# Optimization experiments

Hardware: AMD Instinct MI355X
Metric: run time of the kernel (lower is better)

Reference implementation:

```python
import jax, jax.numpy as jnp
import numpy as np

IMG_H, IMG_W = 1024, 1024
STRIDES = (8, 16, 32, 64, 128)
NUM_CLASSES = 80
CONF_THR = 0.05
IOU_THR = 0.5
MAX_PER_CLASS = 100
MAX_DET = 100
K_CAND = 256  # candidates kept per class before greedy NMS (pre-sort cap)


def build_grids():
    gy, gx, gs = [], [], []
    for s in STRIDES:
        H, W = IMG_H // s, IMG_W // s
        h = jnp.arange(H, dtype=jnp.float32)
        w = jnp.arange(W, dtype=jnp.float32)
        gy_, gx_ = jnp.meshgrid(h, w)  # 'xy' indexing -> shape [W, H], matches tf.meshgrid
        gy.append(gy_.reshape(-1))
        gx.append(gx_.reshape(-1))
        gs.append(jnp.full((W * H,), float(s), dtype=jnp.float32))
    return jnp.concatenate(gy), jnp.concatenate(gx), jnp.concatenate(gs)


def pairwise_iou(b):
    # b: [K,4] as (y1, x1, y2, x2)
    y1, x1, y2, x2 = b[:, 0], b[:, 1], b[:, 2], b[:, 3]
    area = (y2 - y1) * (x2 - x1)
    ih = jnp.maximum(jnp.minimum(y2[:, None], y2[None, :]) - jnp.maximum(y1[:, None], y1[None, :]), 0.0)
    iw = jnp.maximum(jnp.minimum(x2[:, None], x2[None, :]) - jnp.maximum(x1[:, None], x1[None, :]), 0.0)
    inter = ih * iw
    union = area[:, None] + area[None, :] - inter
    return inter / jnp.maximum(union, 1e-8)


def nms_one_class(boxes, scores):
    # boxes [N,4], scores [N] -> (sel_boxes [MAX_PER_CLASS,4], sel_scores [MAX_PER_CLASS])
    top_s, idx = jax.lax.top_k(scores, K_CAND)
    cand = boxes[idx]                       # [K,4]
    valid = top_s > CONF_THR
    iou = jax.lax.stop_gradient(pairwise_iou(cand))  # suppression mask is non-differentiable
    rng = jnp.arange(K_CAND)

    def body(i, keep):
        sup = (iou[i] > IOU_THR) & (rng > i) & keep[i]
        return keep & ~sup

    keep = jax.lax.fori_loop(0, K_CAND, body, valid)
    kept = jnp.where(keep, top_s, 0.0)
    sel_s, sel_i = jax.lax.top_k(kept, MAX_PER_CLASS)
    return cand[sel_i], sel_s


def combined_nms(boxes, scores):
    # per image: boxes [N,4] shared across classes, scores [N,C]
    cls_boxes, cls_scores = jax.vmap(nms_one_class, in_axes=(None, 1))(boxes, scores)
    C = scores.shape[1]
    cls_labels = jnp.broadcast_to(jnp.arange(C, dtype=jnp.float32)[:, None], cls_scores.shape)
    flat_s = cls_scores.reshape(-1)
    flat_b = cls_boxes.reshape(-1, 4)
    flat_l = cls_labels.reshape(-1)
    fin_s, fin_i = jax.lax.top_k(flat_s, MAX_DET)
    fin_b = flat_b[fin_i] * (fin_s > 0.0)[:, None].astype(flat_b.dtype)  # zero pad boxes like TF
    fin_l = flat_l[fin_i]
    return fin_b, fin_l, fin_s


def decode(pred_regs, pred_ctrs, pred_clfs):
    gy, gx, gs = build_grids()
    gy, gx, gs = gy[:, None], gx[:, None], gs[:, None]     # [N,1]
    score = pred_clfs * pred_ctrs                           # [B,N,C]
    x1 = gx - pred_regs[..., 0:1]
    x2 = gx + pred_regs[..., 1:2]
    y1 = gy - pred_regs[..., 2:3]
    y2 = gy + pred_regs[..., 3:4]
    bbox = jnp.concatenate([y1, x1, y2, x2], axis=-1) * gs  # [B,N,4] in image coords
    return jax.vmap(combined_nms)(bbox, score)


def setup_inputs() -> dict:
    key = jax.random.key(0)
    k1, k2, k3 = jax.random.split(key, 3)
    N = sum((IMG_H // s) * (IMG_W // s) for s in STRIDES)  # 21824
    B = 16
    return {
        "pred_regs": jax.random.uniform(k1, (B, N, 4), jnp.float32),
        "pred_ctrs": jax.random.uniform(k2, (B, N, 1), jnp.float32),
        "pred_clfs": jax.random.uniform(k3, (B, N, NUM_CLASSES), jnp.float32),
    }


def reference(pred_regs, pred_ctrs, pred_clfs):
    # returns (final_bboxes [B,100,4], final_labels [B,100] float, final_scores [B,100])
    return decode(pred_regs, pred_ctrs, pred_clfs)
```

## Files before the change

### kernel.cpp

```cpp
#include <hip/hip_runtime.h>
#include <stdint.h>

#pragma clang fp contract(off)

namespace {
constexpr int kN = 21824;
constexpr int kB = 16;
constexpr int kC = 80;
constexpr int kK = 256;
constexpr int kMaxPC = 100;
constexpr int kMaxDet = 100;
constexpr int kBins1 = 2048;
constexpr int kCap = 1536;
constexpr int kQCap = 320;
constexpr int kRows = kB * kC;
constexpr int kTiles = kN / 64;
constexpr int kTPB = 6;
constexpr int kGScan = (kTiles + kTPB - 1) / kTPB;
constexpr int kLCap = 48;
constexpr float kThr = 0.72f;
constexpr double kIouC = 0x1.000001p-1;
}

__device__ __forceinline__ uint64_t make_key(float s, int n) {
  return ((uint64_t)__float_as_uint(s) << 16) | (uint32_t)(0xFFFF - n);
}

__device__ uint32_t block_scan_incl(uint32_t val) {
  __shared__ uint32_t wsum[4];
  int lane = threadIdx.x & 63;
  int wave = threadIdx.x >> 6;
  for (int d = 1; d < 64; d <<= 1) {
    uint32_t t = __shfl_up(val, (unsigned)d, 64);
    if (lane >= d) val += t;
  }
  if (lane == 63) wsum[wave] = val;
  __syncthreads();
  uint32_t off = 0;
  for (int w = 0; w < wave; ++w) off += wsum[w];
  __syncthreads();
  return val + off;
}

struct RegSrc {
  uint64_t k[6];
  int cnt;
  template <class F> __device__ void each(F f) const {
    #pragma unroll
    for (int j = 0; j < 6; ++j)
      if (j < cnt) f(k[j]);
  }
};
struct ColSrc {
  const float* cl;
  const float* ct;
  template <class F> __device__ void each(F f) const {
    for (int n = threadIdx.x; n < kN; n += 256)
      f(make_key(cl[(size_t)n * kC] * ct[n], n));
  }
};
struct ArrSrc {
  const float* s;
  int count;
  template <class F> __device__ void each(F f) const {
    for (int i = threadIdx.x; i < count; i += 256) f(make_key(s[i], i));
  }
};

template <class Src>
__device__ int refine_gather(const Src& src, int K, int cap,
                             uint32_t* hist, uint64_t* cbuf) {
  __shared__ int sel_bin;
  __shared__ uint32_t sel_hd, sel_above, qcnt;
  int tid = threadIdx.x;

  for (int i = tid; i < kBins1; i += 256) hist[i] = 0;
  __syncthreads();
  src.each([&](uint64_t k) { atomicAdd(&hist[(uint32_t)(k >> 37)], 1u); });
  __syncthreads();
  uint32_t krem = (uint32_t)K;
  {
    uint32_t bl[8], v = 0;
    int base = kBins1 - 1 - 8 * tid;
    for (int j = 0; j < 8; ++j) { bl[j] = hist[base - j]; v += bl[j]; }
    uint32_t S = block_scan_incl(v);
    if (S >= krem && (S - v) < krem) {
      uint32_t cum = S - v;
      for (int j = 0; j < 8; ++j) {
        cum += bl[j];
        if (cum >= krem) { sel_bin = base - j; sel_hd = bl[j]; sel_above = cum - bl[j]; break; }
      }
    }
    __syncthreads();
  }
  uint64_t prefix = (uint64_t)sel_bin;
  krem = (uint32_t)K - sel_above;
  uint32_t Sge = ((uint32_t)K - krem) + sel_hd;
  int shift = 37;
  __syncthreads();

  while (Sge > (uint32_t)cap) {
    int w = (shift > 8) ? 8 : shift;
    int ns = shift - w, bins = 1 << w, hs = shift;
    for (int i = tid; i < bins; i += 256) hist[i] = 0;
    __syncthreads();
    uint64_t pfx = prefix;
    src.each([&](uint64_t k) {
      if ((k >> hs) == pfx)
        atomicAdd(&hist[(uint32_t)(k >> ns) & (bins - 1)], 1u);
    });
    __syncthreads();
    uint32_t v = (tid < bins) ? hist[bins - 1 - tid] : 0;
    uint32_t S = block_scan_incl(v);
    if (v && S >= krem && (S - v) < krem) {
      sel_bin = bins - 1 - tid; sel_hd = v; sel_above = S - v;
    }
    __syncthreads();
    prefix = (prefix << w) | (uint32_t)sel_bin;
    krem -= sel_above;
    Sge = ((uint32_t)K - krem) + sel_hd;
    shift = ns;
    __syncthreads();
  }

  uint64_t L = prefix << shift;
  if (tid == 0) qcnt = 0;
  __syncthreads();
  src.each([&](uint64_t k) {
    if (k >= L) {
      uint32_t p = atomicAdd(&qcnt, 1u);
      if (p < (uint32_t)cap) cbuf[p] = k;
    }
  });
  __syncthreads();
  int Scnt = (int)qcnt;
  return Scnt > cap ? cap : Scnt;
}

__global__ __launch_bounds__(256) void zero_cnt_kernel(uint32_t* __restrict__ gcnt) {
  int i = blockIdx.x * 256 + threadIdx.x;
  if (i < kRows) gcnt[i] = 0;
}

__global__ __launch_bounds__(256) void score_scan_kernel(
    const float* __restrict__ clfs, const float* __restrict__ ctrs,
    uint32_t* __restrict__ gcnt, uint64_t* __restrict__ glist) {
  int b = blockIdx.y;
  int t0 = blockIdx.x * kTPB;
  int t1 = t0 + kTPB; if (t1 > kTiles) t1 = kTiles;
  int nbase = t0 * 64;
  int nanch = (t1 - t0) * 64;

  __shared__ uint64_t lbuf[kC][kLCap + 1];
  __shared__ uint32_t lcnt[kC];
  __shared__ uint32_t gbase[kC];
  __shared__ float ct[kTPB * 64];
  int tid = threadIdx.x;
  for (int i = tid; i < kC; i += 256) lcnt[i] = 0;
  for (int i = tid; i < nanch; i += 256) ct[i] = ctrs[(size_t)b * kN + nbase + i];
  __syncthreads();

  const float4* src = (const float4*)(clfs + ((size_t)b * kN + nbase) * kC);
  int n4 = nanch * (kC / 4);
  float4 v = (tid < n4) ? src[tid] : float4{0, 0, 0, 0};
  for (int e = tid; e < n4; e += 256) {
    int en = e + 256;
    float4 vn = (en < n4) ? src[en] : float4{0, 0, 0, 0};
    int a = e / 20;
    int c0 = (e % 20) * 4;
    float cv = ct[a];
    int n = nbase + a;
    float sv[4] = {v.x * cv, v.y * cv, v.z * cv, v.w * cv};
    #pragma unroll
    for (int j = 0; j < 4; ++j) {
      if (sv[j] > kThr) {
        int c = c0 + j;
        uint32_t p = atomicAdd(&lcnt[c], 1u);
        if (p < kLCap) lbuf[c][p] = make_key(sv[j], n);
      }
    }
    v = vn;
  }
  __syncthreads();

  if (tid < kC) {
    uint32_t m = lcnt[tid];
    int row = b * kC + tid;
    if (m > kLCap) {
      atomicAdd(&gcnt[row], (uint32_t)(kCap + 1));
      gbase[tid] = 0xFFFFFFFFu;
    } else {
      gbase[tid] = m ? atomicAdd(&gcnt[row], m) : 0u;
    }
  }
  __syncthreads();

  int lane = tid & 63, wave = tid >> 6;
  for (int c = wave * 20; c < wave * 20 + 20; ++c) {
    uint32_t m = lcnt[c];
    uint32_t base = gbase[c];
    if (base == 0xFFFFFFFFu || m == 0) continue;
    if (m > kLCap) m = kLCap;
    int row = b * kC + c;
    for (uint32_t i = lane; i < m; i += 64) {
      uint32_t p = base + i;
      if (p < kCap) glist[(size_t)row * kCap + p] = lbuf[c][i];
    }
  }
}

__device__ __forceinline__ uint64_t iou_bit(const float4& A, float aA,
                                            const float4& Bx, float aB) {
  float yy1 = fmaxf(A.x, Bx.x);
  float yy2 = fminf(A.z, Bx.z);
  float xx1 = fmaxf(A.y, Bx.y);
  float xx2 = fminf(A.w, Bx.w);
  float ih = fmaxf(yy2 - yy1, 0.0f);
  float iw = fmaxf(xx2 - xx1, 0.0f);
  float inter = ih * iw;
  float un = (aB + aA) - inter;
  float unc = fmaxf(un, 1e-8f);
  return (uint64_t)((double)inter > kIouC * (double)unc);
}

__global__ __launch_bounds__(256) void nms_class_kernel(
    const uint32_t* __restrict__ gcnt, const uint64_t* __restrict__ glist,
    const float* __restrict__ clfs, const float* __restrict__ ctrs,
    const float* __restrict__ regs,
    float* __restrict__ cls_boxes, float* __restrict__ cls_scores) {
  int row = blockIdx.x;
  int b = row / kC, c = row % kC;
  int tid = threadIdx.x;
  int lane = tid & 63, wave = tid >> 6;

  __shared__ union {
    uint32_t hist[kBins1];
    uint64_t supm[kK][4];
  } hu;
  __shared__ uint64_t cbuf[kQCap];
  __shared__ uint64_t skey[kK];
  __shared__ float4 boxf4[kK];
  __shared__ float barea[kK];
  __shared__ uint64_t kinit[4];
  __shared__ uint64_t kfin[4];

  uint32_t cnt = gcnt[row];
  int Scnt;
  if (cnt >= (uint32_t)kK && cnt <= (uint32_t)kCap) {
    RegSrc rs; rs.cnt = 0;
    const uint64_t* gl = glist + (size_t)row * kCap;
    #pragma unroll
    for (int j = 0; j < 6; ++j) {
      int i = tid + j * 256;
      if (i < (int)cnt) { rs.k[j] = gl[i]; rs.cnt = j + 1; }
    }
    Scnt = refine_gather(rs, kK, kQCap, hu.hist, cbuf);
  } else {
    ColSrc cs{clfs + (size_t)b * kN * kC + c, ctrs + (size_t)b * kN};
    Scnt = refine_gather(cs, kK, kQCap, hu.hist, cbuf);
  }

  for (int j = tid; j < Scnt; j += 256) {
    uint64_t kj = cbuf[j];
    int r = 0;
    for (int i = 0; i < Scnt; ++i) r += (cbuf[i] > kj);
    if (r < kK) skey[r] = kj;
  }
  __syncthreads();

  uint64_t myk = skey[tid];
  int n = 0xFFFF - (int)(myk & 0xFFFF);
  float sc_v = __uint_as_float((uint32_t)(myk >> 16));
  int off, hl;
  float sf;
  if (n < 16384)      { off = 0;     hl = 7; sf = 8.f;   }
  else if (n < 20480) { off = 16384; hl = 6; sf = 16.f;  }
  else if (n < 21504) { off = 20480; hl = 5; sf = 32.f;  }
  else if (n < 21760) { off = 21504; hl = 4; sf = 64.f;  }
  else                { off = 21760; hl = 3; sf = 128.f; }
  int kk = n - off;
  float gx = (float)(kk >> hl);
  float gy = (float)(kk & ((1 << hl) - 1));
  const float4 r = ((const float4*)regs)[(size_t)b * kN + n];
  float4 mybox;
  mybox.x = (gy - r.z) * sf;
  mybox.y = (gx - r.x) * sf;
  mybox.z = (gy + r.w) * sf;
  mybox.w = (gx + r.y) * sf;
  float my_a = (mybox.z - mybox.x) * (mybox.w - mybox.y);
  boxf4[tid] = mybox;
  barea[tid] = my_a;
  unsigned long long vm = __ballot(sc_v > 0.05f);
  if (lane == 0) kinit[wave] = vm;
  {
    uint64_t* sp = &hu.supm[0][0];
    #pragma unroll
    for (int q = 0; q < 4; ++q) sp[tid + q * 256] = 0;
  }
  __syncthreads();

  if (tid < 128) {
    int t = tid;
    uint64_t cur = 0;
    int jend = t + 127;
    for (int j = t + 1; j <= jend; ++j) {
      cur |= iou_bit(mybox, my_a, boxf4[j], barea[j]) << (j & 63);
      if ((j & 63) == 63) {
        if (cur) atomicOr((unsigned long long*)&hu.supm[t][j >> 6], cur);
        cur = 0;
      }
    }
    if (cur) atomicOr((unsigned long long*)&hu.supm[t][jend >> 6], cur);
  } else {
    int T = tid - 128;
    float4 bA = boxf4[T]; float aA = barea[T];
    uint64_t cur = 0;
    for (int j = T + 128; j <= 255; ++j) {
      cur |= iou_bit(bA, aA, boxf4[j], barea[j]) << (j & 63);
      if ((j & 63) == 63) {
        if (cur) atomicOr((unsigned long long*)&hu.supm[T][j >> 6], cur);
        cur = 0;
      }
    }
    if (T > 0) {
      int rB = 255 - T;
      float4 bB = boxf4[rB]; float aB = barea[rB];
      for (int j = 256 - T; j <= 255; ++j) {
        cur |= iou_bit(bB, aB, boxf4[j], barea[j]) << (j & 63);
        if ((j & 63) == 63) {
          if (cur) atomicOr((unsigned long long*)&hu.supm[rB][j >> 6], cur);
          cur = 0;
        }
      }
    }
  }
  __syncthreads();

  if (wave == 0) {
    uint64_t kw0 = kinit[0], kw1 = kinit[1], kw2 = kinit[2], kw3 = kinit[3];
    #define NMS_SECTION(W, KW)                                              \
      _Pragma("unroll")                                                     \
      for (int ch = 0; ch < 16; ++ch) {                                     \
        const uint64_t* s0 = hu.supm[(W << 6) + ch * 4 + 0];                \
        const uint64_t* s1 = hu.supm[(W << 6) + ch * 4 + 1];                \
        const uint64_t* s2 = hu.supm[(W << 6) + ch * 4 + 2];                \
        const uint64_t* s3 = hu.supm[(W << 6) + ch * 4 + 3];                \
        uint64_t a0 = s0[0], a1 = s0[1], a2 = s0[2], a3 = s0[3];            \
        uint64_t b0 = s1[0], b1 = s1[1], b2 = s1[2], b3 = s1[3];            \
        uint64_t c0 = s2[0], c1 = s2[1], c2 = s2[2], c3 = s2[3];            \
        uint64_t d0 = s3[0], d1 = s3[1], d2 = s3[2], d3 = s3[3];            \
        if ((KW >> (ch * 4 + 0)) & 1ull) { kw0 &= ~a0; kw1 &= ~a1; kw2 &= ~a2; kw3 &= ~a3; } \
        if ((KW >> (ch * 4 + 1)) & 1ull) { kw0 &= ~b0; kw1 &= ~b1; kw2 &= ~b2; kw3 &= ~b3; } \
        if ((KW >> (ch * 4 + 2)) & 1ull) { kw0 &= ~c0; kw1 &= ~c1; kw2 &= ~c2; kw3 &= ~c3; } \
        if ((KW >> (ch * 4 + 3)) & 1ull) { kw0 &= ~d0; kw1 &= ~d1; kw2 &= ~d2; kw3 &= ~d3; } \
      }
    NMS_SECTION(0, kw0)
    NMS_SECTION(1, kw1)
    NMS_SECTION(2, kw2)
    NMS_SECTION(3, kw3)
    #undef NMS_SECTION
    if (lane == 0) { kfin[0] = kw0; kfin[1] = kw1; kfin[2] = kw2; kfin[3] = kw3; }
  }
  __syncthreads();

  uint64_t kw0 = kfin[0], kw1 = kfin[1], kw2 = kfin[2], kw3 = kfin[3];
  uint64_t ww = (wave == 0) ? kw0 : (wave == 1) ? kw1 : (wave == 2) ? kw2 : kw3;
  bool keptf = (ww >> lane) & 1ull;
  int kept_total = (int)(__popcll(kw0) + __popcll(kw1) +
                         __popcll(kw2) + __popcll(kw3));
  int kept_before = (int)__popcll(ww & ((1ull << lane) - 1ull));
  if (wave > 0) kept_before += (int)__popcll(kw0);
  if (wave > 1) kept_before += (int)__popcll(kw1);
  if (wave > 2) kept_before += (int)__popcll(kw2);

  int rank2 = keptf ? kept_before : (kept_total + tid - kept_before);
  if (rank2 < kMaxPC) {
    float ks = keptf ? sc_v : 0.0f;
    size_t obase = ((size_t)row) * kMaxPC + rank2;
    cls_scores[obase] = ks;
    float* ob = cls_boxes + obase * 4;
    ob[0] = mybox.x; ob[1] = mybox.y; ob[2] = mybox.z; ob[3] = mybox.w;
  }
}

__global__ __launch_bounds__(256) void final_topk_kernel(
    const float* __restrict__ cls_scores, const float* __restrict__ cls_boxes,
    float* __restrict__ out) {
  int b = blockIdx.x;
  int tid = threadIdx.x;
  const int M = kC * kMaxPC;
  __shared__ uint32_t hist[kBins1];
  __shared__ uint64_t cbuf[kQCap];

  ArrSrc as{cls_scores + (size_t)b * M, M};
  int Scnt = refine_gather(as, kMaxDet, kQCap, hist, cbuf);

  for (int j = tid; j < Scnt; j += 256) {
    uint64_t myk = cbuf[j];
    int rank = 0;
    for (int i = 0; i < Scnt; ++i) rank += (cbuf[i] > myk);
    if (rank < kMaxDet) {
      float sv = __uint_as_float((uint32_t)(myk >> 16));
      int f = 0xFFFF - (int)(myk & 0xFFFF);
      int cls = f / 100;
      const float* bp = cls_boxes + ((size_t)b * M + f) * 4;
      float m = (sv > 0.0f) ? 1.0f : 0.0f;
      float* ob = out + ((size_t)b * kMaxDet + rank) * 4;
      ob[0] = bp[0] * m; ob[1] = bp[1] * m; ob[2] = bp[2] * m; ob[3] = bp[3] * m;
      out[(size_t)kB * kMaxDet * 4 + (size_t)b * kMaxDet + rank] = (float)cls;
      out[(size_t)kB * kMaxDet * 5 + (size_t)b * kMaxDet + rank] = sv;
    }
  }
}

extern "C" void kernel_launch(void* const* d_in, const int* in_sizes, int n_in,
                              void* d_out, int out_size, void* d_ws, size_t ws_size,
                              hipStream_t stream) {
  (void)in_sizes; (void)n_in; (void)out_size;
  const float* regs = (const float*)d_in[0];
  const float* ctrs = (const float*)d_in[1];
  const float* clfs = (const float*)d_in[2];
  float* out = (float*)d_out;

  const size_t glB  = (size_t)kRows * kCap * sizeof(uint64_t);
  const size_t cbB  = (size_t)kRows * kMaxPC * 4 * sizeof(float);
  const size_t csB  = (size_t)kRows * kMaxPC * sizeof(float);
  const size_t cntB = 8192;
  if (ws_size < glB + cbB + csB + cntB) return;

  char* p = (char*)d_ws;
  uint64_t* glist   = (uint64_t*)p; p += glB;
  float* cls_boxes  = (float*)p;    p += cbB;
  float* cls_scores = (float*)p;    p += csB;
  uint32_t* gcnt    = (uint32_t*)p;

  zero_cnt_kernel<<<(kRows + 255) / 256, 256, 0, stream>>>(gcnt);
  score_scan_kernel<<<dim3(kGScan, kB), 256, 0, stream>>>(clfs, ctrs, gcnt, glist);
  nms_class_kernel<<<kRows, 256, 0, stream>>>(gcnt, glist, clfs, ctrs, regs,
                                              cls_boxes, cls_scores);
  final_topk_kernel<<<kB, 256, 0, stream>>>(cls_scores, cls_boxes, out);
}
```

Before: 291.3 us.

## Bitonic-sort NMS candidates, single-precision IoU test, vector LDS loads, memset counters

Replaces the O(S^2) rank-counting sort of gathered candidates with a 512-element bitonic sort in a shared buffer unioned with the histogram and suppression matrix. That union frees the separate candidate and sorted-key buffers. The IoU threshold test now uses a float comparison (2*inter > union) instead of a double-precision multiply-compare, and the greedy NMS sweep loads suppression rows as 128-bit vectors. The zeroing kernel is replaced by hipMemsetAsync. The bitonic sort adds many block-wide barriers, and the float IoU test can give different results from the old double-precision check at the exact threshold.

```diff
diff --git a/kernel.cpp b/kernel.cpp
--- a/kernel.cpp
+++ b/kernel.cpp
@@ -13,13 +13,13 @@
 constexpr int kBins1 = 2048;
 constexpr int kCap = 1536;
 constexpr int kQCap = 320;
+constexpr int kSortN = 512;
 constexpr int kRows = kB * kC;
 constexpr int kTiles = kN / 64;
 constexpr int kTPB = 6;
 constexpr int kGScan = (kTiles + kTPB - 1) / kTPB;
 constexpr int kLCap = 48;
 constexpr float kThr = 0.72f;
-constexpr double kIouC = 0x1.000001p-1;
 }
 
 __device__ __forceinline__ uint64_t make_key(float s, int n) {
@@ -135,11 +135,6 @@
   __syncthreads();
   int Scnt = (int)qcnt;
   return Scnt > cap ? cap : Scnt;
-}
-
-__global__ __launch_bounds__(256) void zero_cnt_kernel(uint32_t* __restrict__ gcnt) {
-  int i = blockIdx.x * 256 + threadIdx.x;
-  if (i < kRows) gcnt[i] = 0;
 }
 
 __global__ __launch_bounds__(256) void score_scan_kernel(
@@ -220,7 +215,7 @@
   float inter = ih * iw;
   float un = (aB + aA) - inter;
   float unc = fmaxf(un, 1e-8f);
-  return (uint64_t)((double)inter > kIouC * (double)unc);
+  return (uint64_t)(2.0f * inter > unc);
 }
 
 __global__ __launch_bounds__(256) void nms_class_kernel(
@@ -235,10 +230,9 @@
 
   __shared__ union {
     uint32_t hist[kBins1];
+    uint64_t sortb[kSortN];
     uint64_t supm[kK][4];
   } hu;
-  __shared__ uint64_t cbuf[kQCap];
-  __shared__ uint64_t skey[kK];
   __shared__ float4 boxf4[kK];
   __shared__ float barea[kK];
   __shared__ uint64_t kinit[4];
@@ -254,21 +248,28 @@
       int i = tid + j * 256;
       if (i < (int)cnt) { rs.k[j] = gl[i]; rs.cnt = j + 1; }
     }
-    Scnt = refine_gather(rs, kK, kQCap, hu.hist, cbuf);
+    Scnt = refine_gather(rs, kK, kSortN, hu.hist, hu.sortb);
   } else {
     ColSrc cs{clfs + (size_t)b * kN * kC + c, ctrs + (size_t)b * kN};
-    Scnt = refine_gather(cs, kK, kQCap, hu.hist, cbuf);
-  }
-
-  for (int j = tid; j < Scnt; j += 256) {
-    uint64_t kj = cbuf[j];
-    int r = 0;
-    for (int i = 0; i < Scnt; ++i) r += (cbuf[i] > kj);
-    if (r < kK) skey[r] = kj;
-  }
-  __syncthreads();
-
-  uint64_t myk = skey[tid];
+    Scnt = refine_gather(cs, kK, kSortN, hu.hist, hu.sortb);
+  }
+
+  for (int i = Scnt + tid; i < kSortN; i += 256) hu.sortb[i] = 0;
+  __syncthreads();
+  for (int k2 = 2; k2 <= kSortN; k2 <<= 1) {
+    for (int j = k2 >> 1; j > 0; j >>= 1) {
+      int lo = tid & (j - 1);
+      int i = ((tid ^ lo) << 1) | lo;
+      int p = i | j;
+      uint64_t a = hu.sortb[i], bb = hu.sortb[p];
+      bool sw = ((i & k2) != 0) ? (a > bb) : (a < bb);
+      if (sw) { hu.sortb[i] = bb; hu.sortb[p] = a; }
+      __syncthreads();
+    }
+  }
+  uint64_t myk = hu.sortb[tid];
+  __syncthreads();
+
   int n = 0xFFFF - (int)(myk & 0xFFFF);
   float sc_v = __uint_as_float((uint32_t)(myk >> 16));
   int off, hl;
@@ -341,18 +342,18 @@
     #define NMS_SECTION(W, KW)                                              \
       _Pragma("unroll")                                                     \
       for (int ch = 0; ch < 16; ++ch) {                                     \
-        const uint64_t* s0 = hu.supm[(W << 6) + ch * 4 + 0];                \
-        const uint64_t* s1 = hu.supm[(W << 6) + ch * 4 + 1];                \
-        const uint64_t* s2 = hu.supm[(W << 6) + ch * 4 + 2];                \
-        const uint64_t* s3 = hu.supm[(W << 6) + ch * 4 + 3];                \
-        uint64_t a0 = s0[0], a1 = s0[1], a2 = s0[2], a3 = s0[3];            \
-        uint64_t b0 = s1[0], b1 = s1[1], b2 = s1[2], b3 = s1[3];            \
-        uint64_t c0 = s2[0], c1 = s2[1], c2 = s2[2], c3 = s2[3];            \
-        uint64_t d0 = s3[0], d1 = s3[1], d2 = s3[2], d3 = s3[3];            \
-        if ((KW >> (ch * 4 + 0)) & 1ull) { kw0 &= ~a0; kw1 &= ~a1; kw2 &= ~a2; kw3 &= ~a3; } \
-        if ((KW >> (ch * 4 + 1)) & 1ull) { kw0 &= ~b0; kw1 &= ~b1; kw2 &= ~b2; kw3 &= ~b3; } \
-        if ((KW >> (ch * 4 + 2)) & 1ull) { kw0 &= ~c0; kw1 &= ~c1; kw2 &= ~c2; kw3 &= ~c3; } \
-        if ((KW >> (ch * 4 + 3)) & 1ull) { kw0 &= ~d0; kw1 &= ~d1; kw2 &= ~d2; kw3 &= ~d3; } \
+        const ulonglong2* s0 = (const ulonglong2*)hu.supm[(W << 6) + ch * 4 + 0]; \
+        const ulonglong2* s1 = (const ulonglong2*)hu.supm[(W << 6) + ch * 4 + 1]; \
+        const ulonglong2* s2 = (const ulonglong2*)hu.supm[(W << 6) + ch * 4 + 2]; \
+        const ulonglong2* s3 = (const ulonglong2*)hu.supm[(W << 6) + ch * 4 + 3]; \
+        ulonglong2 aL = s0[0], aH = s0[1];                                  \
+        ulonglong2 bL = s1[0], bH = s1[1];                                  \
+        ulonglong2 cL = s2[0], cH = s2[1];                                  \
+        ulonglong2 dL = s3[0], dH = s3[1];                                  \
+        if ((KW >> (ch * 4 + 0)) & 1ull) { kw0 &= ~aL.x; kw1 &= ~aL.y; kw2 &= ~aH.x; kw3 &= ~aH.y; } \
+        if ((KW >> (ch * 4 + 1)) & 1ull) { kw0 &= ~bL.x; kw1 &= ~bL.y; kw2 &= ~bH.x; kw3 &= ~bH.y; } \
+        if ((KW >> (ch * 4 + 2)) & 1ull) { kw0 &= ~cL.x; kw1 &= ~cL.y; kw2 &= ~cH.x; kw3 &= ~cH.y; } \
+        if ((KW >> (ch * 4 + 3)) & 1ull) { kw0 &= ~dL.x; kw1 &= ~dL.y; kw2 &= ~dH.x; kw3 &= ~dH.y; } \
       }
     NMS_SECTION(0, kw0)
     NMS_SECTION(1, kw1)
@@ -434,7 +435,7 @@
   float* cls_scores = (float*)p;    p += csB;
   uint32_t* gcnt    = (uint32_t*)p;
 
-  zero_cnt_kernel<<<(kRows + 255) / 256, 256, 0, stream>>>(gcnt);
+  hipMemsetAsync(gcnt, 0, (size_t)kRows * sizeof(uint32_t), stream);
   score_scan_kernel<<<dim3(kGScan, kB), 256, 0, stream>>>(clfs, ctrs, gcnt, glist);
   nms_class_kernel<<<kRows, 256, 0, stream>>>(gcnt, glist, clfs, ctrs, regs,
                                               cls_boxes, cls_scores);
```

Result: no change. 285.6 us (-1.9%).
